# Optimization experiments

Measured on AMD Instinct MI355X. Metric: run time of the kernel, lower is better.

The kernel has to match this reference:

```python
import jax, jax.numpy as jnp
import numpy as np

B, STATE_DIM, T = 4096, 24, 8
V, D, LAT = 65536, 64, 128
NL, NH, MAXDIM, MEM = 3, 8, 32, 10
FF = 4 * LAT  # dim_feedforward = latent_dim * 4 = 512


def setup_inputs():
    key = jax.random.key(0)
    ks = jax.random.split(key, 20)
    w = lambda i, shape, s=0.02: (jax.random.normal(ks[i], shape, jnp.float32) * s)
    return {
        "dimension_tokens": jax.random.randint(ks[0], (STATE_DIM, T), 0, V),
        "dimension_traits": jax.random.normal(ks[1], (B, STATE_DIM, 2), jnp.float32),
        "rel_goal": jax.random.normal(ks[2], (B, STATE_DIM), jnp.float32),
        "memory_context": jax.random.normal(ks[3], (B, MEM, D), jnp.float32),
        "token_embedding": w(4, (V, D), 1.0),
        "dim_embedding": w(5, (MAXDIM, D), 1.0),
        "trait_W": w(6, (D, 2)), "trait_b": jnp.zeros((D,), jnp.float32),
        "intent_W": w(7, (D, 1)), "intent_b": jnp.zeros((D,), jnp.float32),
        "cls_token": w(8, (1, 1, D), 1.0),
        "Wqkv": w(9, (NL, 3 * D, D)), "bqkv": jnp.zeros((NL, 3 * D), jnp.float32),
        "Wo": w(10, (NL, D, D)), "bo": jnp.zeros((NL, D), jnp.float32),
        "ln1_g": jnp.ones((NL, D), jnp.float32), "ln1_b": jnp.zeros((NL, D), jnp.float32),
        "W1": w(11, (NL, FF, D)), "b1": jnp.zeros((NL, FF), jnp.float32),
        "W2": w(12, (NL, D, FF)), "b2": jnp.zeros((NL, D), jnp.float32),
        "ln2_g": jnp.ones((NL, D), jnp.float32), "ln2_b": jnp.zeros((NL, D), jnp.float32),
        "out_W": w(13, (LAT, D)), "out_b": jnp.zeros((LAT,), jnp.float32),
        "out_ln_g": jnp.ones((LAT,), jnp.float32), "out_ln_b": jnp.zeros((LAT,), jnp.float32),
    }


def _ln(x, g, b, eps=1e-5):
    m = jnp.mean(x, -1, keepdims=True)
    v = jnp.var(x, -1, keepdims=True)
    return (x - m) * jax.lax.rsqrt(v + eps) * g + b


def _mha(x, Wqkv, bqkv, Wo, bo):
    Bb, S, Dd = x.shape
    hd = Dd // NH
    qkv = x @ Wqkv.T + bqkv
    q, k, v = jnp.split(qkv, 3, axis=-1)
    heads = lambda t: t.reshape(Bb, S, NH, hd).transpose(0, 2, 1, 3)
    q, k, v = heads(q), heads(k), heads(v)
    scores = jnp.einsum('bhqd,bhkd->bhqk', q, k) * np.float32(1.0 / np.sqrt(hd))
    attn = jax.nn.softmax(scores, axis=-1)
    out = jnp.einsum('bhqk,bhkd->bhqd', attn, v).transpose(0, 2, 1, 3).reshape(Bb, S, Dd)
    return out @ Wo.T + bo


def reference(dimension_tokens, dimension_traits, rel_goal, memory_context,
              token_embedding, dim_embedding, trait_W, trait_b, intent_W, intent_b,
              cls_token, Wqkv, bqkv, Wo, bo, ln1_g, ln1_b, W1, b1, W2, b2,
              ln2_g, ln2_b, out_W, out_b, out_ln_g, out_ln_b):
    Bb = rel_goal.shape[0]
    state_dim = rel_goal.shape[-1]
    # fused gather + mean-pool over each dimension's token list: [state_dim, D]
    tok = jnp.mean(token_embedding[dimension_tokens], axis=1)
    pos = dim_embedding[:state_dim]                                   # [state_dim, D]
    trait_e = dimension_traits @ trait_W.T + trait_b                  # [B, state_dim, D]
    intent_e = rel_goal[..., None] @ intent_W.T + intent_b            # [B, state_dim, D]
    seq = tok[None] + pos[None] + trait_e + intent_e                  # [B, state_dim, D]
    cls = jnp.broadcast_to(cls_token, (Bb, 1, D))
    x = jnp.concatenate([cls, seq, memory_context], axis=1)           # [B, 1+state_dim+MEM, D]
    # post-LN (norm_first=False) TransformerEncoder, dropout=0 (eval)
    for l in range(NL):
        x = _ln(x + _mha(x, Wqkv[l], bqkv[l], Wo[l], bo[l]), ln1_g[l], ln1_b[l])
        ff = jax.nn.gelu(x @ W1[l].T + b1[l], approximate=False) @ W2[l].T + b2[l]
        x = _ln(x + ff, ln2_g[l], ln2_b[l])
    situation = _ln(x[:, 0] @ out_W.T + out_b, out_ln_g, out_ln_b)    # [B, LAT]
    situation_sequence = x[:, 1:1 + state_dim]                        # [B, state_dim, D]
    cur = jnp.mean(situation_sequence, axis=1, keepdims=True)
    new_memory = jnp.concatenate([memory_context, cur], axis=1)[:, -MEM:]
    return situation, situation_sequence, new_memory
```

## Files before the change

### kernel.cpp

```cpp
#include <hip/hip_runtime.h>

typedef _Float16 f16;
typedef _Float16 f16x2 __attribute__((ext_vector_type(2)));
typedef _Float16 f16x4 __attribute__((ext_vector_type(4)));
typedef _Float16 f16x8 __attribute__((ext_vector_type(8)));
typedef float floatx4 __attribute__((ext_vector_type(4)));

#define MFMA(a, b, c) __builtin_amdgcn_mfma_f32_16x16x32_f16((a), (b), (c), 0, 0, 0)

constexpr int S = 35;
constexpr int NH = 8;
constexpr int NL = 3;
constexpr int G = 2;
constexpr int RP = 80;
constexpr int MT = 5;
constexpr int XS = 72;
constexpr int HS = 136;
constexpr int BUF = RP * XS;
constexpr int SEQOFF = 4096 * 128;
constexpr int MEMOFF = SEQOFF + 4096 * 24 * 64;

struct Params {
    const int* tok;
    const float *traits, *relg, *mem, *temb, *demb, *traitW, *traitb, *intentW, *intentb, *cls;
    const float *bqkv, *bo, *ln1g, *ln1b, *b1, *b2, *ln2g, *ln2b;
    const float *outW, *outb, *olng, *olnb;
    const f16 *Wqkv, *Wo, *W1, *W2;
    float* out;
};

__global__ void cvt_all(const float* __restrict__ wqkv, const float* __restrict__ wo,
                        const float* __restrict__ w1, const float* __restrict__ w2,
                        f16* __restrict__ dst) {
    int i = (blockIdx.x * 256 + threadIdx.x) * 4;
    const float* src;
    int off;
    if (i < 36864)       { src = wqkv; off = 0; }
    else if (i < 49152)  { src = wo;   off = 36864; }
    else if (i < 147456) { src = w1;   off = 49152; }
    else                 { src = w2;   off = 147456; }
    floatx4 v = *(const floatx4*)&src[i - off];
    f16x4 o;
    o[0] = (f16)v[0]; o[1] = (f16)v[1]; o[2] = (f16)v[2]; o[3] = (f16)v[3];
    *(f16x4*)&dst[i] = o;
}

__device__ inline f16x4 pack4(float a, float b, float c, float d) {
    f16x2 lo = __builtin_bit_cast(f16x2, __builtin_amdgcn_cvt_pkrtz(a, b));
    f16x2 hi = __builtin_bit_cast(f16x2, __builtin_amdgcn_cvt_pkrtz(c, d));
    f16x4 r; r[0] = lo[0]; r[1] = lo[1]; r[2] = hi[0]; r[3] = hi[1];
    return r;
}

__device__ inline float gelu_f(float x) {
    float x3 = x * x * x;
    float y = 1.5957691216f * (x + 0.044715f * x3);
    float z = __expf(-y);
    return x * __builtin_amdgcn_rcpf(1.f + z);
}

__device__ inline void ln_row(const f16* src, f16* dst, const float* g, const float* bb) {
    float v[64];
    float sum = 0.f, sq = 0.f;
#pragma unroll
    for (int kv = 0; kv < 8; ++kv) {
        f16x8 x8 = *(const f16x8*)&src[kv * 8];
#pragma unroll
        for (int e = 0; e < 8; ++e) {
            float f = (float)x8[e];
            v[kv * 8 + e] = f;
            sum += f;
            sq += f * f;
        }
    }
    float mean = sum * (1.f / 64.f);
    float var = sq * (1.f / 64.f) - mean * mean;
    float rs = rsqrtf(var + 1e-5f);
#pragma unroll
    for (int kv = 0; kv < 16; ++kv) {
        floatx4 g4 = *(const floatx4*)&g[kv * 4];
        floatx4 b4 = *(const floatx4*)&bb[kv * 4];
        *(f16x4*)&dst[kv * 4] = pack4((v[kv * 4 + 0] - mean) * rs * g4[0] + b4[0],
                                      (v[kv * 4 + 1] - mean) * rs * g4[1] + b4[1],
                                      (v[kv * 4 + 2] - mean) * rs * g4[2] + b4[2],
                                      (v[kv * 4 + 3] - mean) * rs * g4[3] + b4[3]);
    }
}

__global__ __launch_bounds__(256, 3) void fused_tfm_kernel(Params p) {
    __shared__ __align__(16) f16 xlds[BUF];
    __shared__ __align__(16) f16 scratch[3 * BUF];
    __shared__ float sitlds[G * 128];

    f16* qbuf = scratch;
    f16* kbuf = scratch + BUF;
    f16* vbuf = scratch + 2 * BUF;
    f16* hbuf = scratch;

    const int tid = threadIdx.x;
    const int lane = tid & 63;
    const int w = tid >> 6;
    const int l15 = lane & 15;
    const int quad = lane >> 4;
    const int b0 = blockIdx.x * G;

    float* tokpos = (float*)scratch;
    for (int idx = tid; idx < 24 * 64; idx += 256) {
        int s = idx >> 6, d = idx & 63;
        float a = 0.f;
#pragma unroll
        for (int t = 0; t < 8; ++t) a += p.temb[p.tok[s * 8 + t] * 64 + d];
        tokpos[idx] = a * 0.125f + p.demb[idx] + p.traitb[d] + p.intentb[d];
    }
    __syncthreads();

    for (int idx = tid; idx < G * S * 64; idx += 256) {
        int i = idx / (S * 64);
        int rem = idx - i * S * 64;
        int r = rem >> 6, d = rem & 63;
        int b = b0 + i;
        float v;
        if (r == 0) {
            v = p.cls[d];
        } else if (r <= 24) {
            int s = r - 1;
            v = tokpos[s * 64 + d] + p.traits[b * 48 + s * 2] * p.traitW[d * 2]
                + p.traits[b * 48 + s * 2 + 1] * p.traitW[d * 2 + 1]
                + p.relg[b * 24 + s] * p.intentW[d];
        } else {
            v = p.mem[b * 640 + (r - 25) * 64 + d];
        }
        xlds[(i * S + r) * XS + d] = (f16)v;
    }
    for (int idx = tid; idx < (RP - G * S) * 64; idx += 256) {
        int r = G * S + (idx >> 6), d = idx & 63;
        xlds[r * XS + d] = (f16)0.f;
    }
    __syncthreads();

#pragma unroll 1
    for (int l = 0; l < NL; ++l) {
        const f16* Wqkv_l = p.Wqkv + l * 192 * 64;
        const float* bqkv_l = p.bqkv + l * 192;
        const f16* Wo_l = p.Wo + l * 64 * 64;
        const float* bo_l = p.bo + l * 64;
        const float* ln1g_l = p.ln1g + l * 64;
        const float* ln1b_l = p.ln1b + l * 64;
        const f16* W1_l = p.W1 + l * 512 * 64;
        const float* b1_l = p.b1 + l * 512;
        const f16* W2_l = p.W2 + l * 64 * 512;
        const float* b2_l = p.b2 + l * 64;
        const float* ln2g_l = p.ln2g + l * 64;
        const float* ln2b_l = p.ln2b + l * 64;

        {
            f16x8 xb[MT][2];
#pragma unroll
            for (int m = 0; m < MT; ++m)
#pragma unroll
                for (int kf = 0; kf < 2; ++kf)
                    xb[m][kf] = *(const f16x8*)&xlds[(m * 16 + l15) * XS + kf * 32 + quad * 8];
#pragma unroll
            for (int nt = w; nt < 12; nt += 4) {
                f16x8 wf0 = *(const f16x8*)&Wqkv_l[(nt * 16 + l15) * 64 + quad * 8];
                f16x8 wf1 = *(const f16x8*)&Wqkv_l[(nt * 16 + l15) * 64 + 32 + quad * 8];
                floatx4 bias4 = *(const floatx4*)&bqkv_l[nt * 16 + quad * 4];
                f16* dst = scratch + (nt >> 2) * BUF;
                int oc = (nt & 3) * 16 + quad * 4;
                floatx4 acc[MT];
#pragma unroll
                for (int m = 0; m < MT; ++m) {
                    acc[m] = {0.f, 0.f, 0.f, 0.f};
                    acc[m] = MFMA(wf0, xb[m][0], acc[m]);
                    acc[m] = MFMA(wf1, xb[m][1], acc[m]);
                }
#pragma unroll
                for (int m = 0; m < MT; ++m) {
                    int row = m * 16 + l15;
                    *(f16x4*)&dst[row * XS + oc] =
                        pack4(acc[m][0] + bias4[0], acc[m][1] + bias4[1],
                              acc[m][2] + bias4[2], acc[m][3] + bias4[3]);
                }
            }
        }
        __syncthreads();

        for (int t = tid; t < G * NH * S; t += 256) {
            int i = t / (NH * S);
            int rem = t - i * (NH * S);
            int h = rem / S;
            int q = rem - h * S;
            int rbase = i * S;
            const f16x2* qp = (const f16x2*)&qbuf[(rbase + q) * XS + h * 8];
            f16x2 q0 = qp[0], q1 = qp[1], q2 = qp[2], q3 = qp[3];
            float sc[S];
            float mx = -1e30f;
#pragma unroll
            for (int j = 0; j < S; ++j) {
                const f16x2* kp = (const f16x2*)&kbuf[(rbase + j) * XS + h * 8];
                f16x2 acc2 = q0 * kp[0];
                acc2 = q1 * kp[1] + acc2;
                acc2 = q2 * kp[2] + acc2;
                acc2 = q3 * kp[3] + acc2;
                float s = ((float)acc2[0] + (float)acc2[1]) * 0.35355339059f;
                sc[j] = s;
                mx = fmaxf(mx, s);
            }
            float lsum = 0.f;
#pragma unroll
            for (int j = 0; j < S; ++j) {
                sc[j] = __expf(sc[j] - mx);
                lsum += sc[j];
            }
            f16x2 o0 = {0.f, 0.f}, o1 = {0.f, 0.f}, o2 = {0.f, 0.f}, o3 = {0.f, 0.f};
#pragma unroll
            for (int j = 0; j < S; ++j) {
                const f16x2* vp = (const f16x2*)&vbuf[(rbase + j) * XS + h * 8];
                f16 sj = (f16)sc[j];
                f16x2 s2 = {sj, sj};
                o0 = vp[0] * s2 + o0;
                o1 = vp[1] * s2 + o1;
                o2 = vp[2] * s2 + o2;
                o3 = vp[3] * s2 + o3;
            }
            f16 invh = (f16)__builtin_amdgcn_rcpf(lsum);
            f16x2 inv2 = {invh, invh};
            o0 *= inv2; o1 *= inv2; o2 *= inv2; o3 *= inv2;
            f16x8 ov;
            ov[0] = o0[0]; ov[1] = o0[1]; ov[2] = o1[0]; ov[3] = o1[1];
            ov[4] = o2[0]; ov[5] = o2[1]; ov[6] = o3[0]; ov[7] = o3[1];
            *(f16x8*)&qbuf[(rbase + q) * XS + h * 8] = ov;
        }
        __syncthreads();

        {
            f16x8 ab[MT][2];
#pragma unroll
            for (int m = 0; m < MT; ++m)
#pragma unroll
                for (int kf = 0; kf < 2; ++kf)
                    ab[m][kf] = *(const f16x8*)&qbuf[(m * 16 + l15) * XS + kf * 32 + quad * 8];
            f16x8 wf0 = *(const f16x8*)&Wo_l[(w * 16 + l15) * 64 + quad * 8];
            f16x8 wf1 = *(const f16x8*)&Wo_l[(w * 16 + l15) * 64 + 32 + quad * 8];
            int oc = w * 16 + quad * 4;
            floatx4 bo4 = *(const floatx4*)&bo_l[oc];
            floatx4 oacc[MT];
#pragma unroll
            for (int m = 0; m < MT; ++m) {
                oacc[m] = {0.f, 0.f, 0.f, 0.f};
                oacc[m] = MFMA(wf0, ab[m][0], oacc[m]);
                oacc[m] = MFMA(wf1, ab[m][1], oacc[m]);
            }
#pragma unroll
            for (int m = 0; m < MT; ++m) {
                int row = m * 16 + l15;
                f16x4 res = *(const f16x4*)&xlds[row * XS + oc];
                *(f16x4*)&vbuf[row * XS + oc] =
                    pack4(oacc[m][0] + bo4[0] + (float)res[0],
                          oacc[m][1] + bo4[1] + (float)res[1],
                          oacc[m][2] + bo4[2] + (float)res[2],
                          oacc[m][3] + bo4[3] + (float)res[3]);
            }
        }
        __syncthreads();

        if (tid < G * S) ln_row(&vbuf[tid * XS], &xlds[tid * XS], ln1g_l, ln1b_l);
        __syncthreads();

        {
            f16x8 a2[MT][2];
#pragma unroll
            for (int m = 0; m < MT; ++m)
#pragma unroll
                for (int kf = 0; kf < 2; ++kf)
                    a2[m][kf] = *(const f16x8*)&xlds[(m * 16 + l15) * XS + kf * 32 + quad * 8];
            floatx4 facc[MT];
#pragma unroll
            for (int m = 0; m < MT; ++m) facc[m] = {0.f, 0.f, 0.f, 0.f};

#pragma unroll 1
            for (int c = 0; c < 4; ++c) {
#pragma unroll
                for (int ntl = w; ntl < 8; ntl += 4) {
                    int gc = c * 128 + ntl * 16;
                    f16x8 w1f0 = *(const f16x8*)&W1_l[(gc + l15) * 64 + quad * 8];
                    f16x8 w1f1 = *(const f16x8*)&W1_l[(gc + l15) * 64 + 32 + quad * 8];
                    floatx4 b14 = *(const floatx4*)&b1_l[gc + quad * 4];
                    int oc = ntl * 16 + quad * 4;
                    floatx4 hacc[MT];
#pragma unroll
                    for (int m = 0; m < MT; ++m) {
                        hacc[m] = {0.f, 0.f, 0.f, 0.f};
                        hacc[m] = MFMA(w1f0, a2[m][0], hacc[m]);
                        hacc[m] = MFMA(w1f1, a2[m][1], hacc[m]);
                    }
#pragma unroll
                    for (int m = 0; m < MT; ++m) {
                        int row = m * 16 + l15;
                        *(f16x4*)&hbuf[row * HS + oc] =
                            pack4(gelu_f(hacc[m][0] + b14[0]), gelu_f(hacc[m][1] + b14[1]),
                                  gelu_f(hacc[m][2] + b14[2]), gelu_f(hacc[m][3] + b14[3]));
                    }
                }
                __syncthreads();
                f16x8 w2f[4];
#pragma unroll
                for (int kf = 0; kf < 4; ++kf)
                    w2f[kf] = *(const f16x8*)&W2_l[(w * 16 + l15) * 512 + c * 128 + kf * 32 + quad * 8];
#pragma unroll
                for (int m = 0; m < MT; ++m) {
                    f16x8 h0 = *(const f16x8*)&hbuf[(m * 16 + l15) * HS + 0 + quad * 8];
                    f16x8 h1 = *(const f16x8*)&hbuf[(m * 16 + l15) * HS + 32 + quad * 8];
                    f16x8 h2 = *(const f16x8*)&hbuf[(m * 16 + l15) * HS + 64 + quad * 8];
                    f16x8 h3 = *(const f16x8*)&hbuf[(m * 16 + l15) * HS + 96 + quad * 8];
                    facc[m] = MFMA(w2f[0], h0, facc[m]);
                    facc[m] = MFMA(w2f[1], h1, facc[m]);
                    facc[m] = MFMA(w2f[2], h2, facc[m]);
                    facc[m] = MFMA(w2f[3], h3, facc[m]);
                }
                __syncthreads();
            }

            int oc = w * 16 + quad * 4;
            floatx4 b24 = *(const floatx4*)&b2_l[oc];
#pragma unroll
            for (int m = 0; m < MT; ++m) {
                int row = m * 16 + l15;
                f16x4 res = *(const f16x4*)&xlds[row * XS + oc];
                *(f16x4*)&vbuf[row * XS + oc] =
                    pack4(facc[m][0] + b24[0] + (float)res[0],
                          facc[m][1] + b24[1] + (float)res[1],
                          facc[m][2] + b24[2] + (float)res[2],
                          facc[m][3] + b24[3] + (float)res[3]);
            }
        }
        __syncthreads();

        if (tid < G * S) ln_row(&vbuf[tid * XS], &xlds[tid * XS], ln2g_l, ln2b_l);
        __syncthreads();
    }

    {
        int i = tid >> 7, j = tid & 127;
        const f16* xr = &xlds[(i * S) * XS];
        float s = p.outb[j];
#pragma unroll
        for (int kv = 0; kv < 8; ++kv) {
            f16x8 xv = *(const f16x8*)&xr[kv * 8];
            floatx4 w0 = *(const floatx4*)&p.outW[j * 64 + kv * 8];
            floatx4 w1 = *(const floatx4*)&p.outW[j * 64 + kv * 8 + 4];
#pragma unroll
            for (int e = 0; e < 4; ++e) s += (float)xv[e] * w0[e];
#pragma unroll
            for (int e = 0; e < 4; ++e) s += (float)xv[4 + e] * w1[e];
        }
        sitlds[i * 128 + j] = s;
    }
    __syncthreads();

    if (w < 2) {
        int i = w;
        float v0 = sitlds[i * 128 + lane];
        float v1 = sitlds[i * 128 + 64 + lane];
        float sum = v0 + v1, sq = v0 * v0 + v1 * v1;
#pragma unroll
        for (int off = 32; off >= 1; off >>= 1) {
            sum += __shfl_xor(sum, off, 64);
            sq += __shfl_xor(sq, off, 64);
        }
        float mean = sum * (1.f / 128.f);
        float rs = rsqrtf(sq * (1.f / 128.f) - mean * mean + 1e-5f);
        int b = b0 + i;
        __builtin_nontemporal_store((v0 - mean) * rs * p.olng[lane] + p.olnb[lane],
                                    &p.out[b * 128 + lane]);
        __builtin_nontemporal_store((v1 - mean) * rs * p.olng[64 + lane] + p.olnb[64 + lane],
                                    &p.out[b * 128 + 64 + lane]);
    }

    for (int pp = tid; pp < G * 384; pp += 256) {
        int i = pp / 384;
        int q = pp - i * 384;
        int s = q >> 4, dp = (q & 15) * 4;
        int b = b0 + i;
        f16x4 xv = *(const f16x4*)&xlds[(i * S + 1 + s) * XS + dp];
        floatx4 o = {(float)xv[0], (float)xv[1], (float)xv[2], (float)xv[3]};
        __builtin_nontemporal_store(o, (floatx4*)&p.out[SEQOFF + b * 1536 + s * 64 + dp]);
    }
    for (int pp = tid; pp < G * 144; pp += 256) {
        int i = pp / 144;
        int q = pp - i * 144;
        int mr = q >> 4, dp = (q & 15) * 4;
        int b = b0 + i;
        floatx4 v = *(const floatx4*)&p.mem[b * 640 + (1 + mr) * 64 + dp];
        __builtin_nontemporal_store(v, (floatx4*)&p.out[MEMOFF + b * 640 + mr * 64 + dp]);
    }
    if (tid < G * 64) {
        int i = tid >> 6, d = tid & 63;
        float s = 0.f;
#pragma unroll
        for (int sr = 0; sr < 24; ++sr) s += (float)xlds[(i * S + 1 + sr) * XS + d];
        __builtin_nontemporal_store(s * (1.f / 24.f), &p.out[MEMOFF + (b0 + i) * 640 + 576 + d]);
    }
}

extern "C" void kernel_launch(void* const* d_in, const int* in_sizes, int n_in,
                              void* d_out, int out_size, void* d_ws, size_t ws_size,
                              hipStream_t stream) {
    (void)in_sizes; (void)n_in; (void)out_size; (void)ws_size;

    f16* ws = (f16*)d_ws;
    hipLaunchKernelGGL(cvt_all, dim3(240), dim3(256), 0, stream,
                       (const float*)d_in[11], (const float*)d_in[13],
                       (const float*)d_in[17], (const float*)d_in[19], ws);

    Params p;
    p.tok = (const int*)d_in[0];
    p.traits = (const float*)d_in[1];
    p.relg = (const float*)d_in[2];
    p.mem = (const float*)d_in[3];
    p.temb = (const float*)d_in[4];
    p.demb = (const float*)d_in[5];
    p.traitW = (const float*)d_in[6];
    p.traitb = (const float*)d_in[7];
    p.intentW = (const float*)d_in[8];
    p.intentb = (const float*)d_in[9];
    p.cls = (const float*)d_in[10];
    p.bqkv = (const float*)d_in[12];
    p.bo = (const float*)d_in[14];
    p.ln1g = (const float*)d_in[15];
    p.ln1b = (const float*)d_in[16];
    p.b1 = (const float*)d_in[18];
    p.b2 = (const float*)d_in[20];
    p.ln2g = (const float*)d_in[21];
    p.ln2b = (const float*)d_in[22];
    p.outW = (const float*)d_in[23];
    p.outb = (const float*)d_in[24];
    p.olng = (const float*)d_in[25];
    p.olnb = (const float*)d_in[26];
    p.Wqkv = ws;
    p.Wo = ws + 36864;
    p.W1 = ws + 49152;
    p.W2 = ws + 147456;
    p.out = (float*)d_out;

    hipLaunchKernelGGL(fused_tfm_kernel, dim3(4096 / G), dim3(256), 0, stream, p);
}
```

Baseline: 457.3 us.

## Swizzle LDS layout, hoist token embedding precompute, use exp2 math, raise occupancy

Replaces the padded-stride LDS layout (XS=72, HS=136) with an XOR-swizzled unpadded layout, shrinking shared memory so launch bounds can request 4 blocks per CU instead of 3. The per-block token-embedding averaging moves into an extra block of the weight conversion kernel, so it runs once instead of once per block. GELU and softmax switch to exp2 with constants folded into the scale. Together these aim to cut bank conflicts, redundant gather work and transcendental cost, at the risk of register pressure under the tighter launch bound.

Result: faster. 431.7 us (-5.6%).

```diff
diff --git a/kernel.cpp b/kernel.cpp
--- a/kernel.cpp
+++ b/kernel.cpp
@@ -14,11 +14,17 @@
 constexpr int G = 2;
 constexpr int RP = 80;
 constexpr int MT = 5;
-constexpr int XS = 72;
-constexpr int HS = 136;
-constexpr int BUF = RP * XS;
+constexpr int BUF = RP * 64;
 constexpr int SEQOFF = 4096 * 128;
 constexpr int MEMOFF = SEQOFF + 4096 * 24 * 64;
+constexpr int TOKPOS_OFF = 245760;
+
+__device__ __forceinline__ int sw64(int r, int c) {
+    return (r << 6) + ((((c >> 3) ^ r) & 7) << 3) + (c & 7);
+}
+__device__ __forceinline__ int sw128(int r, int c) {
+    return (r << 7) + ((((c >> 3) ^ (r & 7))) << 3) + (c & 7);
+}
 
 struct Params {
     const int* tok;
@@ -26,12 +32,26 @@
     const float *bqkv, *bo, *ln1g, *ln1b, *b1, *b2, *ln2g, *ln2b;
     const float *outW, *outb, *olng, *olnb;
     const f16 *Wqkv, *Wo, *W1, *W2;
+    const float* tokpos;
     float* out;
 };
 
 __global__ void cvt_all(const float* __restrict__ wqkv, const float* __restrict__ wo,
                         const float* __restrict__ w1, const float* __restrict__ w2,
-                        f16* __restrict__ dst) {
+                        const int* __restrict__ tok, const float* __restrict__ temb,
+                        const float* __restrict__ demb, const float* __restrict__ traitb,
+                        const float* __restrict__ intentb, f16* __restrict__ dst) {
+    if (blockIdx.x == 240) {
+        float* tp = (float*)(dst + TOKPOS_OFF);
+        for (int idx = threadIdx.x; idx < 24 * 64; idx += 256) {
+            int s = idx >> 6, d = idx & 63;
+            float a = 0.f;
+#pragma unroll
+            for (int t = 0; t < 8; ++t) a += temb[tok[s * 8 + t] * 64 + d];
+            tp[idx] = a * 0.125f + demb[idx] + traitb[d] + intentb[d];
+        }
+        return;
+    }
     int i = (blockIdx.x * 256 + threadIdx.x) * 4;
     const float* src;
     int off;
@@ -53,18 +73,19 @@
 }
 
 __device__ inline float gelu_f(float x) {
-    float x3 = x * x * x;
-    float y = 1.5957691216f * (x + 0.044715f * x3);
-    float z = __expf(-y);
+    float x2 = x * x;
+    float u = __builtin_fmaf(x2, 0.044715f, 1.0f);
+    float xm = x * -2.302585f;
+    float z = __builtin_amdgcn_exp2f(xm * u);
     return x * __builtin_amdgcn_rcpf(1.f + z);
 }
 
-__device__ inline void ln_row(const f16* src, f16* dst, const float* g, const float* bb) {
+__device__ inline void ln_row_sw(const f16* buf, f16* dst, int row, const float* g, const float* bb) {
     float v[64];
     float sum = 0.f, sq = 0.f;
 #pragma unroll
     for (int kv = 0; kv < 8; ++kv) {
-        f16x8 x8 = *(const f16x8*)&src[kv * 8];
+        f16x8 x8 = *(const f16x8*)&buf[sw64(row, kv * 8)];
 #pragma unroll
         for (int e = 0; e < 8; ++e) {
             float f = (float)x8[e];
@@ -80,17 +101,17 @@
     for (int kv = 0; kv < 16; ++kv) {
         floatx4 g4 = *(const floatx4*)&g[kv * 4];
         floatx4 b4 = *(const floatx4*)&bb[kv * 4];
-        *(f16x4*)&dst[kv * 4] = pack4((v[kv * 4 + 0] - mean) * rs * g4[0] + b4[0],
-                                      (v[kv * 4 + 1] - mean) * rs * g4[1] + b4[1],
-                                      (v[kv * 4 + 2] - mean) * rs * g4[2] + b4[2],
-                                      (v[kv * 4 + 3] - mean) * rs * g4[3] + b4[3]);
-    }
-}
-
-__global__ __launch_bounds__(256, 3) void fused_tfm_kernel(Params p) {
+        *(f16x4*)&dst[sw64(row, kv * 4)] =
+            pack4((v[kv * 4 + 0] - mean) * rs * g4[0] + b4[0],
+                  (v[kv * 4 + 1] - mean) * rs * g4[1] + b4[1],
+                  (v[kv * 4 + 2] - mean) * rs * g4[2] + b4[2],
+                  (v[kv * 4 + 3] - mean) * rs * g4[3] + b4[3]);
+    }
+}
+
+__global__ __launch_bounds__(256, 4) void fused_tfm_kernel(Params p) {
     __shared__ __align__(16) f16 xlds[BUF];
     __shared__ __align__(16) f16 scratch[3 * BUF];
-    __shared__ float sitlds[G * 128];
 
     f16* qbuf = scratch;
     f16* kbuf = scratch + BUF;
@@ -103,16 +124,6 @@
     const int l15 = lane & 15;
     const int quad = lane >> 4;
     const int b0 = blockIdx.x * G;
-
-    float* tokpos = (float*)scratch;
-    for (int idx = tid; idx < 24 * 64; idx += 256) {
-        int s = idx >> 6, d = idx & 63;
-        float a = 0.f;
-#pragma unroll
-        for (int t = 0; t < 8; ++t) a += p.temb[p.tok[s * 8 + t] * 64 + d];
-        tokpos[idx] = a * 0.125f + p.demb[idx] + p.traitb[d] + p.intentb[d];
-    }
-    __syncthreads();
 
     for (int idx = tid; idx < G * S * 64; idx += 256) {
         int i = idx / (S * 64);
@@ -124,17 +135,17 @@
             v = p.cls[d];
         } else if (r <= 24) {
             int s = r - 1;
-            v = tokpos[s * 64 + d] + p.traits[b * 48 + s * 2] * p.traitW[d * 2]
+            v = p.tokpos[s * 64 + d] + p.traits[b * 48 + s * 2] * p.traitW[d * 2]
                 + p.traits[b * 48 + s * 2 + 1] * p.traitW[d * 2 + 1]
                 + p.relg[b * 24 + s] * p.intentW[d];
         } else {
             v = p.mem[b * 640 + (r - 25) * 64 + d];
         }
-        xlds[(i * S + r) * XS + d] = (f16)v;
+        xlds[sw64(i * S + r, d)] = (f16)v;
     }
     for (int idx = tid; idx < (RP - G * S) * 64; idx += 256) {
         int r = G * S + (idx >> 6), d = idx & 63;
-        xlds[r * XS + d] = (f16)0.f;
+        xlds[sw64(r, d)] = (f16)0.f;
     }
     __syncthreads();
 
@@ -159,7 +170,7 @@
             for (int m = 0; m < MT; ++m)
 #pragma unroll
                 for (int kf = 0; kf < 2; ++kf)
-                    xb[m][kf] = *(const f16x8*)&xlds[(m * 16 + l15) * XS + kf * 32 + quad * 8];
+                    xb[m][kf] = *(const f16x8*)&xlds[sw64(m * 16 + l15, kf * 32 + quad * 8)];
 #pragma unroll
             for (int nt = w; nt < 12; nt += 4) {
                 f16x8 wf0 = *(const f16x8*)&Wqkv_l[(nt * 16 + l15) * 64 + quad * 8];
@@ -177,7 +188,7 @@
 #pragma unroll
                 for (int m = 0; m < MT; ++m) {
                     int row = m * 16 + l15;
-                    *(f16x4*)&dst[row * XS + oc] =
+                    *(f16x4*)&dst[sw64(row, oc)] =
                         pack4(acc[m][0] + bias4[0], acc[m][1] + bias4[1],
                               acc[m][2] + bias4[2], acc[m][3] + bias4[3]);
                 }
@@ -191,31 +202,31 @@
             int h = rem / S;
             int q = rem - h * S;
             int rbase = i * S;
-            const f16x2* qp = (const f16x2*)&qbuf[(rbase + q) * XS + h * 8];
+            const f16x2* qp = (const f16x2*)&qbuf[sw64(rbase + q, h * 8)];
             f16x2 q0 = qp[0], q1 = qp[1], q2 = qp[2], q3 = qp[3];
             float sc[S];
             float mx = -1e30f;
 #pragma unroll
             for (int j = 0; j < S; ++j) {
-                const f16x2* kp = (const f16x2*)&kbuf[(rbase + j) * XS + h * 8];
+                const f16x2* kp = (const f16x2*)&kbuf[sw64(rbase + j, h * 8)];
                 f16x2 acc2 = q0 * kp[0];
                 acc2 = q1 * kp[1] + acc2;
                 acc2 = q2 * kp[2] + acc2;
                 acc2 = q3 * kp[3] + acc2;
-                float s = ((float)acc2[0] + (float)acc2[1]) * 0.35355339059f;
+                float s = ((float)acc2[0] + (float)acc2[1]) * 0.51006982f;
                 sc[j] = s;
                 mx = fmaxf(mx, s);
             }
             float lsum = 0.f;
 #pragma unroll
             for (int j = 0; j < S; ++j) {
-                sc[j] = __expf(sc[j] - mx);
+                sc[j] = __builtin_amdgcn_exp2f(sc[j] - mx);
                 lsum += sc[j];
             }
             f16x2 o0 = {0.f, 0.f}, o1 = {0.f, 0.f}, o2 = {0.f, 0.f}, o3 = {0.f, 0.f};
 #pragma unroll
             for (int j = 0; j < S; ++j) {
-                const f16x2* vp = (const f16x2*)&vbuf[(rbase + j) * XS + h * 8];
+                const f16x2* vp = (const f16x2*)&vbuf[sw64(rbase + j, h * 8)];
                 f16 sj = (f16)sc[j];
                 f16x2 s2 = {sj, sj};
                 o0 = vp[0] * s2 + o0;
@@ -229,7 +240,7 @@
             f16x8 ov;
             ov[0] = o0[0]; ov[1] = o0[1]; ov[2] = o1[0]; ov[3] = o1[1];
             ov[4] = o2[0]; ov[5] = o2[1]; ov[6] = o3[0]; ov[7] = o3[1];
-            *(f16x8*)&qbuf[(rbase + q) * XS + h * 8] = ov;
+            *(f16x8*)&qbuf[sw64(rbase + q, h * 8)] = ov;
         }
         __syncthreads();
 
@@ -239,7 +250,7 @@
             for (int m = 0; m < MT; ++m)
 #pragma unroll
                 for (int kf = 0; kf < 2; ++kf)
-                    ab[m][kf] = *(const f16x8*)&qbuf[(m * 16 + l15) * XS + kf * 32 + quad * 8];
+                    ab[m][kf] = *(const f16x8*)&qbuf[sw64(m * 16 + l15, kf * 32 + quad * 8)];
             f16x8 wf0 = *(const f16x8*)&Wo_l[(w * 16 + l15) * 64 + quad * 8];
             f16x8 wf1 = *(const f16x8*)&Wo_l[(w * 16 + l15) * 64 + 32 + quad * 8];
             int oc = w * 16 + quad * 4;
@@ -254,8 +265,8 @@
 #pragma unroll
             for (int m = 0; m < MT; ++m) {
                 int row = m * 16 + l15;
-                f16x4 res = *(const f16x4*)&xlds[row * XS + oc];
-                *(f16x4*)&vbuf[row * XS + oc] =
+                f16x4 res = *(const f16x4*)&xlds[sw64(row, oc)];
+                *(f16x4*)&vbuf[sw64(row, oc)] =
                     pack4(oacc[m][0] + bo4[0] + (float)res[0],
                           oacc[m][1] + bo4[1] + (float)res[1],
                           oacc[m][2] + bo4[2] + (float)res[2],
@@ -264,7 +275,7 @@
         }
         __syncthreads();
 
-        if (tid < G * S) ln_row(&vbuf[tid * XS], &xlds[tid * XS], ln1g_l, ln1b_l);
+        if (tid < G * S) ln_row_sw(vbuf, xlds, tid, ln1g_l, ln1b_l);
         __syncthreads();
 
         {
@@ -273,7 +284,7 @@
             for (int m = 0; m < MT; ++m)
 #pragma unroll
                 for (int kf = 0; kf < 2; ++kf)
-                    a2[m][kf] = *(const f16x8*)&xlds[(m * 16 + l15) * XS + kf * 32 + quad * 8];
+                    a2[m][kf] = *(const f16x8*)&xlds[sw64(m * 16 + l15, kf * 32 + quad * 8)];
             floatx4 facc[MT];
 #pragma unroll
             for (int m = 0; m < MT; ++m) facc[m] = {0.f, 0.f, 0.f, 0.f};
@@ -297,7 +308,7 @@
 #pragma unroll
                     for (int m = 0; m < MT; ++m) {
                         int row = m * 16 + l15;
-                        *(f16x4*)&hbuf[row * HS + oc] =
+                        *(f16x4*)&hbuf[sw128(row, oc)] =
                             pack4(gelu_f(hacc[m][0] + b14[0]), gelu_f(hacc[m][1] + b14[1]),
                                   gelu_f(hacc[m][2] + b14[2]), gelu_f(hacc[m][3] + b14[3]));
                     }
@@ -309,10 +320,10 @@
                     w2f[kf] = *(const f16x8*)&W2_l[(w * 16 + l15) * 512 + c * 128 + kf * 32 + quad * 8];
 #pragma unroll
                 for (int m = 0; m < MT; ++m) {
-                    f16x8 h0 = *(const f16x8*)&hbuf[(m * 16 + l15) * HS + 0 + quad * 8];
-                    f16x8 h1 = *(const f16x8*)&hbuf[(m * 16 + l15) * HS + 32 + quad * 8];
-                    f16x8 h2 = *(const f16x8*)&hbuf[(m * 16 + l15) * HS + 64 + quad * 8];
-                    f16x8 h3 = *(const f16x8*)&hbuf[(m * 16 + l15) * HS + 96 + quad * 8];
+                    f16x8 h0 = *(const f16x8*)&hbuf[sw128(m * 16 + l15, 0 + quad * 8)];
+                    f16x8 h1 = *(const f16x8*)&hbuf[sw128(m * 16 + l15, 32 + quad * 8)];
+                    f16x8 h2 = *(const f16x8*)&hbuf[sw128(m * 16 + l15, 64 + quad * 8)];
+                    f16x8 h3 = *(const f16x8*)&hbuf[sw128(m * 16 + l15, 96 + quad * 8)];
                     facc[m] = MFMA(w2f[0], h0, facc[m]);
                     facc[m] = MFMA(w2f[1], h1, facc[m]);
                     facc[m] = MFMA(w2f[2], h2, facc[m]);
@@ -326,8 +337,8 @@
 #pragma unroll
             for (int m = 0; m < MT; ++m) {
                 int row = m * 16 + l15;
-                f16x4 res = *(const f16x4*)&xlds[row * XS + oc];
-                *(f16x4*)&vbuf[row * XS + oc] =
+                f16x4 res = *(const f16x4*)&xlds[sw64(row, oc)];
+                *(f16x4*)&vbuf[sw64(row, oc)] =
                     pack4(facc[m][0] + b24[0] + (float)res[0],
                           facc[m][1] + b24[1] + (float)res[1],
                           facc[m][2] + b24[2] + (float)res[2],
@@ -336,17 +347,17 @@
         }
         __syncthreads();
 
-        if (tid < G * S) ln_row(&vbuf[tid * XS], &xlds[tid * XS], ln2g_l, ln2b_l);
-        __syncthreads();
-    }
-
+        if (tid < G * S) ln_row_sw(vbuf, xlds, tid, ln2g_l, ln2b_l);
+        __syncthreads();
+    }
+
+    float* sitlds = (float*)scratch;
     {
         int i = tid >> 7, j = tid & 127;
-        const f16* xr = &xlds[(i * S) * XS];
         float s = p.outb[j];
 #pragma unroll
         for (int kv = 0; kv < 8; ++kv) {
-            f16x8 xv = *(const f16x8*)&xr[kv * 8];
+            f16x8 xv = *(const f16x8*)&xlds[sw64(i * S, kv * 8)];
             floatx4 w0 = *(const floatx4*)&p.outW[j * 64 + kv * 8];
             floatx4 w1 = *(const floatx4*)&p.outW[j * 64 + kv * 8 + 4];
 #pragma unroll
@@ -382,7 +393,7 @@
         int q = pp - i * 384;
         int s = q >> 4, dp = (q & 15) * 4;
         int b = b0 + i;
-        f16x4 xv = *(const f16x4*)&xlds[(i * S + 1 + s) * XS + dp];
+        f16x4 xv = *(const f16x4*)&xlds[sw64(i * S + 1 + s, dp)];
         floatx4 o = {(float)xv[0], (float)xv[1], (float)xv[2], (float)xv[3]};
         __builtin_nontemporal_store(o, (floatx4*)&p.out[SEQOFF + b * 1536 + s * 64 + dp]);
     }
@@ -398,7 +409,7 @@
         int i = tid >> 6, d = tid & 63;
         float s = 0.f;
 #pragma unroll
-        for (int sr = 0; sr < 24; ++sr) s += (float)xlds[(i * S + 1 + sr) * XS + d];
+        for (int sr = 0; sr < 24; ++sr) s += (float)xlds[sw64(i * S + 1 + sr, d)];
         __builtin_nontemporal_store(s * (1.f / 24.f), &p.out[MEMOFF + (b0 + i) * 640 + 576 + d]);
     }
 }
@@ -409,9 +420,12 @@
     (void)in_sizes; (void)n_in; (void)out_size; (void)ws_size;
 
     f16* ws = (f16*)d_ws;
-    hipLaunchKernelGGL(cvt_all, dim3(240), dim3(256), 0, stream,
+    hipLaunchKernelGGL(cvt_all, dim3(241), dim3(256), 0, stream,
                        (const float*)d_in[11], (const float*)d_in[13],
-                       (const float*)d_in[17], (const float*)d_in[19], ws);
+                       (const float*)d_in[17], (const float*)d_in[19],
+                       (const int*)d_in[0], (const float*)d_in[4],
+                       (const float*)d_in[5], (const float*)d_in[7],
+                       (const float*)d_in[9], ws);
 
     Params p;
     p.tok = (const int*)d_in[0];
@@ -441,6 +455,7 @@
     p.Wo = ws + 36864;
     p.W1 = ws + 49152;
     p.W2 = ws + 147456;
+    p.tokpos = (const float*)(ws + TOKPOS_OFF);
     p.out = (float*)d_out;
 
     hipLaunchKernelGGL(fused_tfm_kernel, dim3(4096 / G), dim3(256), 0, stream, p);
```
